# Performance work log

Hardware: AMD Instinct MI355X
Metric: run time of the kernel (lower is better)

## Reference

```python
import jax, jax.numpy as jnp
import numpy as np

N_NODES = 50000   # gnn_nodes_num
N_EDGES = 800000  # avg degree 16
HIDDEN = 64       # hidden_channels
BATCH_Y = 2048    # |y|


def setup_inputs() -> dict:
    key = jax.random.key(0)
    ks = jax.random.split(key, 16)
    s = 0.05
    H = HIDDEN
    return {
        "x": jnp.arange(N_NODES, dtype=jnp.int32),
        "edge_index": jax.random.randint(ks[0], (2, N_EDGES), 0, N_NODES, dtype=jnp.int32),
        "y": jax.random.randint(ks[1], (BATCH_Y,), 0, N_NODES, dtype=jnp.int32),
        # learned params
        "emb": jax.random.normal(ks[2], (N_NODES, H), dtype=jnp.float32) * s,
        "Wq": jax.random.normal(ks[3], (H, H), dtype=jnp.float32) * s,
        "bq": jnp.zeros((H,), dtype=jnp.float32),
        "Wk": jax.random.normal(ks[4], (H, H), dtype=jnp.float32) * s,
        "bk": jnp.zeros((H,), dtype=jnp.float32),
        "Wv": jax.random.normal(ks[5], (H, H), dtype=jnp.float32) * s,
        "bv": jnp.zeros((H,), dtype=jnp.float32),
        "Ws": jax.random.normal(ks[6], (H, H), dtype=jnp.float32) * s,  # root/skip lin
        "bs": jnp.zeros((H,), dtype=jnp.float32),
        "W1": jax.random.normal(ks[7], (H, N_NODES), dtype=jnp.float32) * s,
        "b1": jnp.zeros((N_NODES,), dtype=jnp.float32),
    }


def reference(x, edge_index, y, emb, Wq, bq, Wk, bk, Wv, bv, Ws, bs, W1, b1):
    H = Wq.shape[1]
    h = emb[x]                                  # [N, H] embedding lookup
    src, dst = edge_index[0], edge_index[1]

    # TransformerConv (heads=1, root_weight=True): per-node projections
    q = h @ Wq + bq                             # [N, H]
    k = h @ Wk + bk
    v = h @ Wv + bv

    # attention logits per edge, softmax grouped by destination node
    logits = jnp.sum(q[dst] * k[src], axis=-1) / jnp.sqrt(jnp.float32(H))  # [E]
    m = jax.ops.segment_max(logits, dst, num_segments=N_NODES)             # [N]
    e = jnp.exp(logits - m[dst])
    denom = jax.ops.segment_sum(e, dst, num_segments=N_NODES)              # [N]
    alpha = e / denom[dst]                                                 # [E]

    agg = jax.ops.segment_sum(alpha[:, None] * v[src], dst, num_segments=N_NODES)
    out = agg + h @ Ws + bs                     # [N, H] GAT output

    # for each node u: sum of out[dst] over edges with src == u  (vectorized
    # form of the original per-y boolean-mask loop), then gather at y
    neigh = jax.ops.segment_sum(out[dst], src, num_segments=N_NODES)       # [N, H]
    new_x = neigh[y]                            # [B, H]

    return jax.nn.softmax(new_x @ W1 + b1, axis=-1)  # [B, N]
```

## Files before the change

### kernel.cpp

```cpp
#include <hip/hip_runtime.h>
#include <math.h>

#define NN 50000
#define NE 800000
#define HH 64
#define NB 2048
#define NPAD 53248
#define NST 64
#define TPS 13
#define LOG2E 1.4426950408889634f

typedef __attribute__((ext_vector_type(8))) short bf16x8;
typedef __attribute__((ext_vector_type(4))) float f32x4;

__device__ inline ushort f2bf(float f) {
  uint u = __float_as_uint(f);
  uint r = (u + 0x7fffu + ((u >> 16) & 1u)) >> 16;
  return (ushort)r;
}
__device__ inline float bf2f(uint u) { return __uint_as_float(u << 16); }

__device__ inline float fexp2(float x) {
#if __has_builtin(__builtin_amdgcn_exp2f)
  return __builtin_amdgcn_exp2f(x);
#else
  return exp2f(x);
#endif
}

__global__ __launch_bounds__(256) void k_prep(
    const float* __restrict__ W1, const float* __restrict__ b1,
    const float* __restrict__ Wq, const float* __restrict__ Wk,
    const float* __restrict__ Wv, const float* __restrict__ Ws,
    ushort* __restrict__ W1T, float* __restrict__ eb, ushort* __restrict__ WT,
    int* cnt_d, int* cnt_s, char* flag, char* ymark)
{
  int i = blockIdx.x * 256 + threadIdx.x;
  if (i < NN) { cnt_d[i] = 0; cnt_s[i] = 0; flag[i] = 0; ymark[i] = 0; }
  if (i < 4 * HH * HH) {
    int m = i >> 12, rem = i & 4095;
    int c = rem >> 6, kk = rem & 63;
    const float* W = (m == 0) ? Wq : (m == 1) ? Wk : (m == 2) ? Wv : Ws;
    WT[i] = f2bf(W[kk * HH + c]);
  }
  if (i < NPAD) {
    eb[i] = (i < NN) ? __expf(b1[i]) : 0.f;
    uint4 o[8];
    ushort* op = (ushort*)o;
    if (i < NN) {
#pragma unroll
      for (int k = 0; k < HH; ++k) op[k] = f2bf(W1[(size_t)k * NN + i] * LOG2E);
    } else {
#pragma unroll
      for (int k = 0; k < HH; ++k) op[k] = 0;
    }
    uint4* dst = (uint4*)(W1T + (size_t)i * HH);
#pragma unroll
    for (int j = 0; j < 8; ++j) dst[j] = o[j];
  }
}

__global__ __launch_bounds__(256) void k_mark(const int* __restrict__ y,
                                              char* __restrict__ ymark) {
  int i = blockIdx.x * 256 + threadIdx.x;
  if (i < NB) ymark[y[i]] = 1;
}

__global__ __launch_bounds__(256) void k_hist(const int* __restrict__ src,
                                              const int* __restrict__ dst,
                                              const char* __restrict__ ymark,
                                              int* cnt_s, int* cnt_d,
                                              char* __restrict__ flag,
                                              int* __restrict__ rank_d,
                                              int* __restrict__ rank_s) {
  int e = blockIdx.x * 256 + threadIdx.x;
  if (e < NE) {
    int s = src[e], d = dst[e];
    rank_d[e] = atomicAdd(&cnt_d[d], 1);
    if (ymark[s]) {
      rank_s[e] = atomicAdd(&cnt_s[s], 1);
      flag[d] = 1;
    } else {
      rank_s[e] = -1;
    }
  }
}

__global__ __launch_bounds__(1024) void k_scan(
    const int* __restrict__ cnt_d, int* indptr_d,
    const int* __restrict__ cnt_s, int* indptr_s)
{
  const int* cnt = (blockIdx.x == 0) ? cnt_d : cnt_s;
  int* indptr    = (blockIdx.x == 0) ? indptr_d : indptr_s;
  __shared__ int sums[1024];
  const int CH = (NN + 1023) / 1024;
  int t = threadIdx.x;
  int begin = t * CH;
  int end = begin + CH; if (end > NN) end = NN;
  int s = 0;
  for (int i = begin; i < end; ++i) s += cnt[i];
  sums[t] = s;
  __syncthreads();
  for (int off = 1; off < 1024; off <<= 1) {
    int val = (t >= off) ? sums[t - off] : 0;
    __syncthreads();
    sums[t] += val;
    __syncthreads();
  }
  int prefix = (t == 0) ? 0 : sums[t - 1];
  for (int i = begin; i < end; ++i) {
    indptr[i] = prefix;
    prefix += cnt[i];
  }
  if (t == 0) indptr[NN] = sums[1023];
}

__global__ __launch_bounds__(256) void k_qkvs(
    const int* __restrict__ x, const float* __restrict__ emb,
    const ushort* __restrict__ WT,
    const float* __restrict__ bq, const float* __restrict__ bk,
    const float* __restrict__ bv, const float* __restrict__ bs,
    ushort* __restrict__ qb, ushort* __restrict__ kb, ushort* __restrict__ vb,
    float* __restrict__ hs)
{
  int l = threadIdx.x & 63, w = threadIdx.x >> 6;
  int lr = l & 15, lk = l >> 4;
  int r0 = blockIdx.x * 64;
  const ushort* wt = WT + w * HH * HH;
  const float* B = (w == 0) ? bq : (w == 1) ? bk : (w == 2) ? bv : bs;

  bf16x8 b[2][4];
#pragma unroll
  for (int kt = 0; kt < 2; ++kt)
#pragma unroll
    for (int nt = 0; nt < 4; ++nt)
      b[kt][nt] = *(const bf16x8*)(wt + (nt * 16 + lr) * HH + kt * 32 + lk * 8);

  bf16x8 a[2][4];
#pragma unroll
  for (int mt = 0; mt < 4; ++mt) {
    int row = r0 + mt * 16 + lr;
    int g = (row < NN) ? x[row] : 0;
    const float* hp = emb + (size_t)g * HH;
#pragma unroll
    for (int kt = 0; kt < 2; ++kt) {
      float4 f0 = *(const float4*)(hp + kt * 32 + lk * 8);
      float4 f1 = *(const float4*)(hp + kt * 32 + lk * 8 + 4);
      bf16x8 af;
      af[0] = f2bf(f0.x); af[1] = f2bf(f0.y); af[2] = f2bf(f0.z); af[3] = f2bf(f0.w);
      af[4] = f2bf(f1.x); af[5] = f2bf(f1.y); af[6] = f2bf(f1.z); af[7] = f2bf(f1.w);
      a[kt][mt] = af;
    }
  }

  f32x4 acc[4][4];
  const f32x4 z4 = {0.f, 0.f, 0.f, 0.f};
#pragma unroll
  for (int mt = 0; mt < 4; ++mt)
#pragma unroll
    for (int nt = 0; nt < 4; ++nt) acc[mt][nt] = z4;
#pragma unroll
  for (int kt = 0; kt < 2; ++kt)
#pragma unroll
    for (int mt = 0; mt < 4; ++mt)
#pragma unroll
      for (int nt = 0; nt < 4; ++nt)
        acc[mt][nt] = __builtin_amdgcn_mfma_f32_16x16x32_bf16(a[kt][mt], b[kt][nt], acc[mt][nt], 0, 0, 0);

  if (w < 3) {
    ushort* Db = (w == 0) ? qb : (w == 1) ? kb : vb;
#pragma unroll
    for (int mt = 0; mt < 4; ++mt)
#pragma unroll
      for (int r = 0; r < 4; ++r) {
        int row = r0 + mt * 16 + lk * 4 + r;
        if (row < NN) {
#pragma unroll
          for (int nt = 0; nt < 4; ++nt) {
            int c = nt * 16 + lr;
            Db[(size_t)row * HH + c] = f2bf(acc[mt][nt][r] + B[c]);
          }
        }
      }
  } else {
#pragma unroll
    for (int mt = 0; mt < 4; ++mt)
#pragma unroll
      for (int r = 0; r < 4; ++r) {
        int row = r0 + mt * 16 + lk * 4 + r;
        if (row < NN) {
#pragma unroll
          for (int nt = 0; nt < 4; ++nt) {
            int c = nt * 16 + lr;
            hs[(size_t)row * HH + c] = acc[mt][nt][r] + B[c];
          }
        }
      }
  }
}

__global__ __launch_bounds__(256) void k_efill(
    const int* __restrict__ src, const int* __restrict__ dst,
    const ushort* __restrict__ qb, const ushort* __restrict__ kb,
    const char* __restrict__ flag,
    const int* __restrict__ indptr_s, const int* __restrict__ indptr_d,
    const int* __restrict__ rank_d, const int* __restrict__ rank_s,
    int* __restrict__ dstlist_s, int2* __restrict__ slot_d)
{
  int gid = blockIdx.x * 256 + threadIdx.x;
  int e = gid >> 3;
  int lane = gid & 7;
  if (e >= NE) return;
  int s = src[e], d = dst[e];
  bool fd = flag[d];
  float p = 0.f;
  if (fd) {
    uint4 qa = *(const uint4*)(qb + (size_t)d * HH + lane * 8);
    uint4 ka = *(const uint4*)(kb + (size_t)s * HH + lane * 8);
    p += bf2f(qa.x & 0xffffu) * bf2f(ka.x & 0xffffu) + bf2f(qa.x >> 16) * bf2f(ka.x >> 16);
    p += bf2f(qa.y & 0xffffu) * bf2f(ka.y & 0xffffu) + bf2f(qa.y >> 16) * bf2f(ka.y >> 16);
    p += bf2f(qa.z & 0xffffu) * bf2f(ka.z & 0xffffu) + bf2f(qa.z >> 16) * bf2f(ka.z >> 16);
    p += bf2f(qa.w & 0xffffu) * bf2f(ka.w & 0xffffu) + bf2f(qa.w >> 16) * bf2f(ka.w >> 16);
    p += __shfl_xor(p, 4);
    p += __shfl_xor(p, 2);
    p += __shfl_xor(p, 1);
  }
  if (lane == 0) {
    if (fd) {
      int pd = indptr_d[d] + rank_d[e];
      int2 sl; sl.x = s; sl.y = __float_as_int(p * (0.125f * LOG2E));
      slot_d[pd] = sl;
    }
    int rs = rank_s[e];
    if (rs >= 0) dstlist_s[indptr_s[s] + rs] = d;
  }
}

__global__ __launch_bounds__(256) void k_agg(
    const int* __restrict__ indptr_d, const int2* __restrict__ slot_d,
    const ushort* __restrict__ vb, const char* __restrict__ flag,
    float* __restrict__ hs)
{
  int w = (blockIdx.x * 256 + threadIdx.x) >> 6;
  int lane = threadIdx.x & 63;
  if (w >= NN) return;
  if (!flag[w]) return;
  int beg = indptr_d[w], end = indptr_d[w + 1];
  if (beg == end) return;
  float den = 0.f, acc = 0.f;
  for (int j = beg; j < end; ++j) {
    int2 sl = slot_d[j];
    float p = fexp2(__int_as_float(sl.y));
    den += p;
    acc = fmaf(p, bf2f((uint)vb[(size_t)sl.x * HH + lane]), acc);
  }
  hs[(size_t)w * HH + lane] += acc / den;
}

__global__ __launch_bounds__(256) void k_newx(
    const int* __restrict__ y, const int* __restrict__ indptr_s,
    const int* __restrict__ dstlist_s, const float* __restrict__ outn,
    ushort* __restrict__ nxbf)
{
  int w = (blockIdx.x * 256 + threadIdx.x) >> 6;
  int lane = threadIdx.x & 63;
  if (w >= NB) return;
  int u = y[w];
  int beg = indptr_s[u], end = indptr_s[u + 1];
  float acc = 0.f;
  for (int j = beg; j < end; ++j) acc += outn[(size_t)dstlist_s[j] * HH + lane];
  nxbf[w * HH + lane] = f2bf(acc);
}

#define LOADA(A, t) do { int bn0_ = (t) * 64;                                    \
  _Pragma("unroll") for (int kt = 0; kt < 2; ++kt)                               \
  _Pragma("unroll") for (int nt = 0; nt < 4; ++nt)                               \
    A[kt][nt] = *(const bf16x8*)(w1t + (size_t)(bn0_ + nt * 16 + lr) * HH + kt * 32 + lk * 8); \
} while (0)

#define MFMA8(A, acc) do {                                                       \
  _Pragma("unroll") for (int kt = 0; kt < 2; ++kt)                               \
  _Pragma("unroll") for (int nt = 0; nt < 4; ++nt)                               \
    acc[nt] = __builtin_amdgcn_mfma_f32_16x16x32_bf16(A[kt][nt], bm[kt], acc[nt], 0, 0, 0); \
} while (0)

#define PROCA(A, t) do { int bn0_ = (t) * 64;                                    \
  f32x4 acc[4];                                                                  \
  _Pragma("unroll") for (int nt = 0; nt < 4; ++nt) acc[nt] = z4;                 \
  MFMA8(A, acc);                                                                 \
  _Pragma("unroll") for (int nt = 0; nt < 4; ++nt) {                             \
    int n0 = bn0_ + nt * 16 + lk * 4;                                            \
    f32x4 e4 = *(const f32x4*)(eb + n0);                                         \
    _Pragma("unroll") for (int r = 0; r < 4; ++r)                                \
      se += fexp2(acc[nt][r]) * e4[r];                                           \
  }                                                                              \
} while (0)

#define PROCB(A, t) do { int bn0_ = (t) * 64;                                    \
  f32x4 acc[4];                                                                  \
  _Pragma("unroll") for (int nt = 0; nt < 4; ++nt) acc[nt] = z4;                 \
  MFMA8(A, acc);                                                                 \
  _Pragma("unroll") for (int nt = 0; nt < 4; ++nt) {                             \
    int n0 = bn0_ + nt * 16 + lk * 4;                                            \
    f32x4 e4 = *(const f32x4*)(eb + n0);                                         \
    f32x4 vx;                                                                    \
    _Pragma("unroll") for (int r = 0; r < 4; ++r)                                \
      vx[r] = fexp2(acc[nt][r]) * e4[r] * sv;                                    \
    if (n0 < NN)                                                                 \
      __builtin_nontemporal_store(vx, (f32x4*)(out + (size_t)(r0 + lr) * NN + n0)); \
  }                                                                              \
} while (0)

__global__ __launch_bounds__(256, 4) void k_finA(
    const ushort* __restrict__ nxbf, const ushort* __restrict__ w1t,
    const float* __restrict__ eb, float* __restrict__ Spart)
{
  int tid = threadIdx.x;
  int l = tid & 63, w = tid >> 6;
  int lr = l & 15, lk = l >> 4;
  int b = blockIdx.x;
  int st = (b & 7) * 8 + ((b >> 3) & 7);
  int r0 = ((b >> 6) * 4 + w) * 16;
  int tile0 = st * TPS;
  const f32x4 z4 = {0.f, 0.f, 0.f, 0.f};

  bf16x8 bm[2];
#pragma unroll
  for (int kt = 0; kt < 2; ++kt)
    bm[kt] = *(const bf16x8*)(nxbf + (size_t)(r0 + lr) * HH + kt * 32 + lk * 8);

  float se = 0.f;
  {
    bf16x8 A0[2][4], A1[2][4];
    LOADA(A0, tile0);
#pragma unroll
    for (int i = 0; i < 6; ++i) {
      LOADA(A1, tile0 + 2 * i + 1);
      PROCA(A0, tile0 + 2 * i);
      LOADA(A0, tile0 + 2 * i + 2);
      PROCA(A1, tile0 + 2 * i + 1);
    }
    PROCA(A0, tile0 + 12);
  }
  se += __shfl_xor(se, 16);
  se += __shfl_xor(se, 32);
  if (lk == 0) Spart[(r0 + lr) * NST + st] = se;
}

__global__ __launch_bounds__(256) void k_sinv(const float* __restrict__ Spart,
                                              float* __restrict__ Sinv) {
  int r = blockIdx.x * 256 + threadIdx.x;
  if (r < NB) {
    float s = 0.f;
#pragma unroll
    for (int j = 0; j < NST; ++j) s += Spart[r * NST + j];
    Sinv[r] = 1.0f / s;
  }
}

__global__ __launch_bounds__(256, 4) void k_finB(
    const ushort* __restrict__ nxbf, const ushort* __restrict__ w1t,
    const float* __restrict__ eb, const float* __restrict__ Sinv,
    float* __restrict__ out)
{
  int tid = threadIdx.x;
  int l = tid & 63, w = tid >> 6;
  int lr = l & 15, lk = l >> 4;
  int b = blockIdx.x;
  int st = (b & 7) * 8 + ((b >> 3) & 7);
  int r0 = ((b >> 6) * 4 + w) * 16;
  int tile0 = st * TPS;
  const f32x4 z4 = {0.f, 0.f, 0.f, 0.f};

  bf16x8 bm[2];
#pragma unroll
  for (int kt = 0; kt < 2; ++kt)
    bm[kt] = *(const bf16x8*)(nxbf + (size_t)(r0 + lr) * HH + kt * 32 + lk * 8);

  float sv = Sinv[r0 + lr];

  {
    bf16x8 A0[2][4], A1[2][4];
    LOADA(A0, tile0);
#pragma unroll
    for (int i = 0; i < 6; ++i) {
      LOADA(A1, tile0 + 2 * i + 1);
      PROCB(A0, tile0 + 2 * i);
      LOADA(A0, tile0 + 2 * i + 2);
      PROCB(A1, tile0 + 2 * i + 1);
    }
    PROCB(A0, tile0 + 12);
  }
}

extern "C" void kernel_launch(void* const* d_in, const int* in_sizes, int n_in,
                              void* d_out, int out_size, void* d_ws, size_t ws_size,
                              hipStream_t stream)
{
  const int* x   = (const int*)d_in[0];
  const int* src = (const int*)d_in[1];
  const int* dst = src + NE;
  const int* y   = (const int*)d_in[2];
  const float* emb = (const float*)d_in[3];
  const float* Wq = (const float*)d_in[4];  const float* bq = (const float*)d_in[5];
  const float* Wk = (const float*)d_in[6];  const float* bk = (const float*)d_in[7];
  const float* Wv = (const float*)d_in[8];  const float* bv = (const float*)d_in[9];
  const float* Ws = (const float*)d_in[10]; const float* bs = (const float*)d_in[11];
  const float* W1 = (const float*)d_in[12]; const float* b1 = (const float*)d_in[13];
  float* out = (float*)d_out;

  char* wsb = (char*)d_ws;
  ushort* nxbf  = (ushort*)wsb;
  ushort* w1t   = (ushort*)(wsb + 262144);
  float*  Spart = (float*)(wsb + 7077888);
  float*  Sinv  = (float*)(wsb + 7602176);
  float*  eb    = (float*)(wsb + 7610368);
  const size_t PERS  = 7823360;
  const size_t BIGSZ = 46400000;
  char* big = (ws_size >= PERS + BIGSZ) ? (wsb + PERS) : (char*)d_out;
  ushort* qb     = (ushort*)(big + 0);
  ushort* kb     = (ushort*)(big + 6400000);
  ushort* vb     = (ushort*)(big + 12800000);
  float*  hs     = (float*)(big + 19200000);
  int2*   slot_d = (int2*)(big + 32000000);
  int* dstlist_s = (int*)(big + 38400000);
  int* rank_d    = (int*)(big + 38700000);
  int* rank_s    = (int*)(big + 41900000);
  int* cnt_d     = (int*)(big + 45100000);
  int* cnt_s     = (int*)(big + 45300000);
  int* indptr_d  = (int*)(big + 45500000);
  int* indptr_s  = (int*)(big + 45700064);
  char* flag     = (char*)(big + 45900128);
  char* ymark    = (char*)(big + 45950176);
  ushort* WT     = (ushort*)(big + 46000224);

  k_prep<<<dim3(224), dim3(256), 0, stream>>>(W1, b1, Wq, Wk, Wv, Ws, w1t, eb, WT,
                                              cnt_d, cnt_s, flag, ymark);
  k_mark<<<dim3(8), dim3(256), 0, stream>>>(y, ymark);
  k_hist<<<dim3(3125), dim3(256), 0, stream>>>(src, dst, ymark, cnt_s, cnt_d,
                                               flag, rank_d, rank_s);
  k_scan<<<dim3(2), dim3(1024), 0, stream>>>(cnt_d, indptr_d, cnt_s, indptr_s);
  k_qkvs<<<dim3(782), dim3(256), 0, stream>>>(x, emb, WT, bq, bk, bv, bs,
                                              qb, kb, vb, hs);
  k_efill<<<dim3(25000), dim3(256), 0, stream>>>(src, dst, qb, kb, flag,
                                                 indptr_s, indptr_d, rank_d, rank_s,
                                                 dstlist_s, slot_d);
  k_agg<<<dim3(12500), dim3(256), 0, stream>>>(indptr_d, slot_d, vb, flag, hs);
  k_newx<<<dim3(512), dim3(256), 0, stream>>>(y, indptr_s, dstlist_s, hs, nxbf);
  k_finA<<<dim3(2048), dim3(256), 0, stream>>>(nxbf, w1t, eb, Spart);
  k_sinv<<<dim3(8), dim3(256), 0, stream>>>(Spart, Sinv);
  k_finB<<<dim3(2048), dim3(256), 0, stream>>>(nxbf, w1t, eb, Sinv, out);
}
```

Before: 499.6 us.

## Store unnormalized exp logits in fp16 workspace instead of recomputing GEMM

```diff
diff --git a/kernel.cpp b/kernel.cpp
--- a/kernel.cpp
+++ b/kernel.cpp
@@ -311,6 +311,23 @@
   }                                                                              \
 } while (0)
 
+#define PROCZ(A, t) do { int bn0_ = (t) * 64;                                    \
+  f32x4 acc[4];                                                                  \
+  _Pragma("unroll") for (int nt = 0; nt < 4; ++nt) acc[nt] = z4;                 \
+  MFMA8(A, acc);                                                                 \
+  _Pragma("unroll") for (int nt = 0; nt < 4; ++nt) {                             \
+    int n0 = bn0_ + nt * 16 + lk * 4;                                            \
+    f32x4 e4 = *(const f32x4*)(eb + n0);                                         \
+    union { _Float16 h[4]; uint2 u; } pk;                                        \
+    _Pragma("unroll") for (int r = 0; r < 4; ++r) {                              \
+      float ur = fexp2(acc[nt][r]) * e4[r];                                      \
+      se += ur;                                                                  \
+      pk.h[r] = (_Float16)ur;                                                    \
+    }                                                                            \
+    *(uint2*)(zb + (size_t)(r0 + lr) * NPAD + n0) = pk.u;                        \
+  }                                                                              \
+} while (0)
+
 __global__ __launch_bounds__(256, 4) void k_finA(
     const ushort* __restrict__ nxbf, const ushort* __restrict__ w1t,
     const float* __restrict__ eb, float* __restrict__ Spart)
@@ -347,21 +364,10 @@
   if (lk == 0) Spart[(r0 + lr) * NST + st] = se;
 }
 
-__global__ __launch_bounds__(256) void k_sinv(const float* __restrict__ Spart,
-                                              float* __restrict__ Sinv) {
-  int r = blockIdx.x * 256 + threadIdx.x;
-  if (r < NB) {
-    float s = 0.f;
-#pragma unroll
-    for (int j = 0; j < NST; ++j) s += Spart[r * NST + j];
-    Sinv[r] = 1.0f / s;
-  }
-}
-
-__global__ __launch_bounds__(256, 4) void k_finB(
+__global__ __launch_bounds__(256, 4) void k_finZ(
     const ushort* __restrict__ nxbf, const ushort* __restrict__ w1t,
-    const float* __restrict__ eb, const float* __restrict__ Sinv,
-    float* __restrict__ out)
+    const float* __restrict__ eb, ushort* __restrict__ zb,
+    float* __restrict__ Spart)
 {
   int tid = threadIdx.x;
   int l = tid & 63, w = tid >> 6;
@@ -377,6 +383,54 @@
   for (int kt = 0; kt < 2; ++kt)
     bm[kt] = *(const bf16x8*)(nxbf + (size_t)(r0 + lr) * HH + kt * 32 + lk * 8);
 
+  float se = 0.f;
+  {
+    bf16x8 A0[2][4], A1[2][4];
+    LOADA(A0, tile0);
+#pragma unroll
+    for (int i = 0; i < 6; ++i) {
+      LOADA(A1, tile0 + 2 * i + 1);
+      PROCZ(A0, tile0 + 2 * i);
+      LOADA(A0, tile0 + 2 * i + 2);
+      PROCZ(A1, tile0 + 2 * i + 1);
+    }
+    PROCZ(A0, tile0 + 12);
+  }
+  se += __shfl_xor(se, 16);
+  se += __shfl_xor(se, 32);
+  if (lk == 0) Spart[(r0 + lr) * NST + st] = se;
+}
+
+__global__ __launch_bounds__(256) void k_sinv(const float* __restrict__ Spart,
+                                              float* __restrict__ Sinv) {
+  int r = blockIdx.x * 256 + threadIdx.x;
+  if (r < NB) {
+    float s = 0.f;
+#pragma unroll
+    for (int j = 0; j < NST; ++j) s += Spart[r * NST + j];
+    Sinv[r] = 1.0f / s;
+  }
+}
+
+__global__ __launch_bounds__(256, 4) void k_finB(
+    const ushort* __restrict__ nxbf, const ushort* __restrict__ w1t,
+    const float* __restrict__ eb, const float* __restrict__ Sinv,
+    float* __restrict__ out)
+{
+  int tid = threadIdx.x;
+  int l = tid & 63, w = tid >> 6;
+  int lr = l & 15, lk = l >> 4;
+  int b = blockIdx.x;
+  int st = (b & 7) * 8 + ((b >> 3) & 7);
+  int r0 = ((b >> 6) * 4 + w) * 16;
+  int tile0 = st * TPS;
+  const f32x4 z4 = {0.f, 0.f, 0.f, 0.f};
+
+  bf16x8 bm[2];
+#pragma unroll
+  for (int kt = 0; kt < 2; ++kt)
+    bm[kt] = *(const bf16x8*)(nxbf + (size_t)(r0 + lr) * HH + kt * 32 + lk * 8);
+
   float sv = Sinv[r0 + lr];
 
   {
@@ -390,6 +444,28 @@
       PROCB(A1, tile0 + 2 * i + 1);
     }
     PROCB(A0, tile0 + 12);
+  }
+}
+
+__global__ __launch_bounds__(256) void k_finN(
+    const ushort* __restrict__ zb, const float* __restrict__ Sinv,
+    float* __restrict__ out)
+{
+  int r = blockIdx.x;
+  float sv = Sinv[r];
+  const ushort* zr = zb + (size_t)r * NPAD;
+  float* orow = out + (size_t)r * NN;
+  for (int c0 = threadIdx.x * 8; c0 < NN; c0 += 2048) {
+    uint4 zv = *(const uint4*)(zr + c0);
+    const _Float16* hp = (const _Float16*)&zv;
+    f32x4 v0, v1;
+#pragma unroll
+    for (int j = 0; j < 4; ++j) {
+      v0[j] = (float)hp[j] * sv;
+      v1[j] = (float)hp[4 + j] * sv;
+    }
+    *(f32x4*)(orow + c0) = v0;
+    *(f32x4*)(orow + c0 + 4) = v1;
   }
 }
 
@@ -415,9 +491,14 @@
   float*  Spart = (float*)(wsb + 7077888);
   float*  Sinv  = (float*)(wsb + 7602176);
   float*  eb    = (float*)(wsb + 7610368);
-  const size_t PERS  = 7823360;
-  const size_t BIGSZ = 46400000;
-  char* big = (ws_size >= PERS + BIGSZ) ? (wsb + PERS) : (char*)d_out;
+  const size_t PERS   = 7823360;
+  const size_t ZSZ    = (size_t)NB * NPAD * 2;
+  const size_t PERS_Z = PERS + ZSZ;
+  const size_t BIGSZ  = 46400000;
+  bool zpath = ws_size >= PERS_Z + BIGSZ;
+  ushort* zb = (ushort*)(wsb + PERS);
+  char* big = zpath ? (wsb + PERS_Z)
+                    : ((ws_size >= PERS + BIGSZ) ? (wsb + PERS) : (char*)d_out);
   ushort* qb     = (ushort*)(big + 0);
   ushort* kb     = (ushort*)(big + 6400000);
   ushort* vb     = (ushort*)(big + 12800000);
@@ -447,7 +528,13 @@
                                                  dstlist_s, slot_d);
   k_agg<<<dim3(12500), dim3(256), 0, stream>>>(indptr_d, slot_d, vb, flag, hs);
   k_newx<<<dim3(512), dim3(256), 0, stream>>>(y, indptr_s, dstlist_s, hs, nxbf);
-  k_finA<<<dim3(2048), dim3(256), 0, stream>>>(nxbf, w1t, eb, Spart);
-  k_sinv<<<dim3(8), dim3(256), 0, stream>>>(Spart, Sinv);
-  k_finB<<<dim3(2048), dim3(256), 0, stream>>>(nxbf, w1t, eb, Sinv, out);
-}
+  if (zpath) {
+    k_finZ<<<dim3(2048), dim3(256), 0, stream>>>(nxbf, w1t, eb, zb, Spart);
+    k_sinv<<<dim3(8), dim3(256), 0, stream>>>(Spart, Sinv);
+    k_finN<<<dim3(2048), dim3(256), 0, stream>>>(zb, Sinv, out);
+  } else {
+    k_finA<<<dim3(2048), dim3(256), 0, stream>>>(nxbf, w1t, eb, Spart);
+    k_sinv<<<dim3(8), dim3(256), 0, stream>>>(Spart, Sinv);
+    k_finB<<<dim3(2048), dim3(256), 0, stream>>>(nxbf, w1t, eb, Sinv, out);
+  }
+}
```

After: 531.2 us. +6.3%, slower.
